# Performance work log

Measured on AMD Instinct MI355X. Metric: run time of the kernel, lower is better.

The kernel has to match this reference:

```python
import jax, jax.numpy as jnp
import numpy as np

B, NQ, HW, D, H = 4, 100, 4096, 1024, 16
HD = D // H  # head dim = 64
EPS = 1e-5
NEG = -1e9


def layernorm(x, g, b):
    mu = jnp.mean(x, axis=-1, keepdims=True)
    var = jnp.mean(jnp.square(x - mu), axis=-1, keepdims=True)
    return (x - mu) * jax.lax.rsqrt(var + EPS) * g + b


def setup_inputs() -> dict:
    key = jax.random.key(0)
    ks = jax.random.split(key, 6)
    scale = 0.02
    return {
        "q": jax.random.normal(ks[0], (B, NQ, D), dtype=jnp.float32),
        "kv": jax.random.normal(ks[1], (B, HW, D), dtype=jnp.float32),
        "mask": jax.random.randint(ks[2], (B, NQ, HW), 0, 2, dtype=jnp.int32),
        "in_proj_w": scale * jax.random.normal(ks[3], (3 * D, D), dtype=jnp.float32),
        "in_proj_b": jnp.zeros((3 * D,), dtype=jnp.float32),
        "out_w": scale * jax.random.normal(ks[4], (D, D), dtype=jnp.float32),
        "out_b": jnp.zeros((D,), dtype=jnp.float32),
        "g_q": jnp.ones((D,), dtype=jnp.float32),
        "b_q": jnp.zeros((D,), dtype=jnp.float32),
        "g_kv": jnp.ones((D,), dtype=jnp.float32),
        "b_kv": jnp.zeros((D,), dtype=jnp.float32),
    }


def reference(q, kv, mask, in_proj_w, in_proj_b, out_w, out_b, g_q, b_q, g_kv, b_kv):
    qn = layernorm(q, g_q, b_q)      # [B,NQ,D]
    kvn = layernorm(kv, g_kv, b_kv)  # [B,HW,D]

    # nn.MultiheadAttention fused in-projection: rows [Wq; Wk; Wv]
    Wq, Wk, Wv = jnp.split(in_proj_w, 3, axis=0)
    bq, bk, bv = jnp.split(in_proj_b, 3, axis=0)
    qp = (qn @ Wq.T + bq).reshape(B, NQ, H, HD)
    kp = (kvn @ Wk.T + bk).reshape(B, HW, H, HD)
    vp = (kvn @ Wv.T + bv).reshape(B, HW, H, HD)

    scores = jnp.einsum("bqhd,bkhd->bhqk", qp, kp) / jnp.sqrt(jnp.float32(HD))

    # Per-query key mask; a query with an all-zero mask attends everywhere
    # (original code sets key_padding_mask=None when kpm.all()).
    allowed = mask.astype(bool)                                   # [B,NQ,HW]
    has_any = jnp.any(allowed, axis=-1, keepdims=True)
    eff = jnp.where(has_any, allowed, True)
    scores = jnp.where(eff[:, None, :, :], scores, NEG)

    attn = jax.nn.softmax(scores, axis=-1)                        # [B,H,NQ,HW]
    ctx = jnp.einsum("bhqk,bkhd->bqhd", attn, vp).reshape(B, NQ, D)
    return ctx @ out_w.T + out_b
```

## Files before the change

### kernel.cpp

```cpp
#include <hip/hip_runtime.h>
#include <math.h>
#include <stdint.h>

#define B_    4
#define NQ_   100
#define HW_   4096
#define D_    1024
#define H_    16
#define HD_   64
#define NCH_  2
#define KCH_  (HW_/NCH_)
#define NT_   (KCH_/128)
#define QT_   32
#define MP_   512

typedef __attribute__((ext_vector_type(8))) short short8;
typedef __attribute__((ext_vector_type(8))) unsigned short ushort8v;
typedef __attribute__((ext_vector_type(4))) float f32x4;

__device__ __forceinline__ unsigned short f2bf(float f) {
    unsigned int u = __float_as_uint(f);
    u += 0x7fffu + ((u >> 16) & 1u);
    return (unsigned short)(u >> 16);
}
__device__ __forceinline__ float bf2f(unsigned short h) {
    return __uint_as_float(((unsigned int)h) << 16);
}

__device__ __forceinline__ void gl2lds16(const void* g, void* l) {
    typedef __attribute__((address_space(1))) unsigned int gu32;
    typedef __attribute__((address_space(3))) unsigned int lu32;
    __builtin_amdgcn_global_load_lds(
        reinterpret_cast<gu32*>(reinterpret_cast<uintptr_t>(g)),
        reinterpret_cast<lu32*>(reinterpret_cast<uintptr_t>(l)),
        16, 0, 0);
}

#define VMCNT0() asm volatile("s_waitcnt vmcnt(0)" ::: "memory")
#define BARRIER() do { __builtin_amdgcn_s_barrier(); \
                       __builtin_amdgcn_sched_barrier(0); } while (0)

__device__ __forceinline__ void ln_row(
    const float* __restrict__ x, const float* __restrict__ g,
    const float* __restrict__ be, unsigned short* __restrict__ y,
    int row, int real_rows, int lane)
{
    unsigned short* yr = y + (size_t)row * D_;
    if (row >= real_rows) {
        #pragma unroll
        for (int k = 0; k < 4; ++k)
            *reinterpret_cast<ushort4*>(yr + lane*4 + k*256) = make_ushort4(0,0,0,0);
        return;
    }
    const float* xr = x + (size_t)row * D_;
    float4 v[4];
    float s = 0.f, ss = 0.f;
    #pragma unroll
    for (int k = 0; k < 4; ++k) {
        v[k] = *reinterpret_cast<const float4*>(xr + lane*4 + k*256);
        s  += v[k].x + v[k].y + v[k].z + v[k].w;
        ss += v[k].x*v[k].x + v[k].y*v[k].y + v[k].z*v[k].z + v[k].w*v[k].w;
    }
    #pragma unroll
    for (int o = 1; o < 64; o <<= 1) {
        s  += __shfl_xor(s,  o);
        ss += __shfl_xor(ss, o);
    }
    const float mu = s * (1.0f / D_);
    const float rs = rsqrtf(ss * (1.0f / D_) - mu*mu + 1e-5f);
    #pragma unroll
    for (int k = 0; k < 4; ++k) {
        const float4 gg = *reinterpret_cast<const float4*>(g  + lane*4 + k*256);
        const float4 bb = *reinterpret_cast<const float4*>(be + lane*4 + k*256);
        ushort4 o;
        o.x = f2bf((v[k].x - mu) * rs * gg.x + bb.x);
        o.y = f2bf((v[k].y - mu) * rs * gg.y + bb.y);
        o.z = f2bf((v[k].z - mu) * rs * gg.z + bb.z);
        o.w = f2bf((v[k].w - mu) * rs * gg.w + bb.w);
        *reinterpret_cast<ushort4*>(yr + lane*4 + k*256) = o;
    }
}

__global__ __launch_bounds__(256) void prep_kernel(
    const float* __restrict__ kv,   const float* __restrict__ g_kv,
    const float* __restrict__ b_kv, unsigned short* __restrict__ kvn,
    const float* __restrict__ qf,   const float* __restrict__ g_q,
    const float* __restrict__ b_q,  unsigned short* __restrict__ qn,
    const float* __restrict__ in_w, unsigned short* __restrict__ wfull,
    const float* __restrict__ out_w, unsigned short* __restrict__ wout,
    const int* __restrict__ mask,   unsigned int* __restrict__ mp)
{
    __shared__ int red[4];
    const int bid = blockIdx.x, tid = threadIdx.x;

    if (bid < 4096) {
        ln_row(kv, g_kv, b_kv, kvn, bid*4 + (tid >> 6), B_*HW_, tid & 63);
    } else if (bid < 7168) {
        const int i = (bid - 4096)*256 + tid;
        const float4 v = reinterpret_cast<const float4*>(in_w)[i];
        ushort4 o;
        o.x = f2bf(v.x); o.y = f2bf(v.y); o.z = f2bf(v.z); o.w = f2bf(v.w);
        reinterpret_cast<ushort4*>(wfull)[i] = o;
    } else if (bid < 8192) {
        const int row = bid - 7168;
        const float4 v = reinterpret_cast<const float4*>(out_w + (size_t)row * D_)[tid];
        ushort4 hi, lo;
        hi.x = f2bf(v.x); hi.y = f2bf(v.y); hi.z = f2bf(v.z); hi.w = f2bf(v.w);
        lo.x = f2bf(v.x - bf2f(hi.x)); lo.y = f2bf(v.y - bf2f(hi.y));
        lo.z = f2bf(v.z - bf2f(hi.z)); lo.w = f2bf(v.w - bf2f(hi.w));
        unsigned short* yr = wout + (size_t)row * 3072;
        reinterpret_cast<ushort4*>(yr)[tid]        = hi;
        reinterpret_cast<ushort4*>(yr + 1024)[tid] = hi;
        reinterpret_cast<ushort4*>(yr + 2048)[tid] = lo;
    } else if (bid < 8704) {
        const int mblk = bid - 8192;
        const int qrow = mblk & 127, mb = mblk >> 7;
        unsigned int word = 0;
        if (qrow < NQ_ && tid < 128) {
            const int4* mr = reinterpret_cast<const int4*>(
                mask + ((size_t)(mb*NQ_ + qrow))*HW_ + tid*32);
            #pragma unroll
            for (int j = 0; j < 8; ++j) {
                const int4 v = mr[j];
                word |= (v.x!=0 ? 1u:0u) << (4*j);
                word |= (v.y!=0 ? 1u:0u) << (4*j+1);
                word |= (v.z!=0 ? 1u:0u) << (4*j+2);
                word |= (v.w!=0 ? 1u:0u) << (4*j+3);
            }
        }
        const int wany = __any(word != 0) ? 1 : 0;
        if ((tid & 63) == 0) red[tid >> 6] = wany;
        __syncthreads();
        const int hasany = red[0] | red[1] | red[2] | red[3];
        if (tid < 128)
            mp[((size_t)(mb*128 + qrow))*128 + tid] = hasany ? word : 0xFFFFFFFFu;
    } else {
        ln_row(qf, g_q, b_q, qn, (bid - 8704)*4 + (tid >> 6), B_*NQ_, tid & 63);
    }
}

__global__ __launch_bounds__(512, 4) void gemm_kv_kernel(
    const unsigned short* __restrict__ A, const unsigned short* __restrict__ Wb,
    const float* __restrict__ bias, unsigned short* __restrict__ kp,
    unsigned short* __restrict__ vt,
    const unsigned short* __restrict__ qA, const unsigned short* __restrict__ qW,
    float* __restrict__ P)
{
    extern __shared__ __align__(16) unsigned short lds[];

    const int tid  = threadIdx.x;
    const int wave = tid >> 6;
    const int lane = tid & 63;
    const int lr   = lane & 15, quad = lane >> 4;

    if (blockIdx.x >= 1024) {
        const int bid2 = blockIdx.x - 1024;
        const int bn = bid2 & 15, bm = (bid2 >> 4) & 7, sk = bid2 >> 7;
        unsigned short* As = lds;
        unsigned short* Bs = lds + 2048;

        const int r0 = (tid & 255) >> 2;
        const int xs = (r0 & 3) ^ ((r0 >> 2) & 3);
        const int kc = (tid & 3) ^ xs;
        const unsigned short* ap = qA + (size_t)(bm*64 + r0)*1024 + sk*128 + kc*8;
        const unsigned short* bp = qW + (size_t)(bn*64 + r0)*1024 + sk*128 + kc*8;
        unsigned short* asd = As + (wave & 3)*512;
        unsigned short* bsd = Bs + (wave & 3)*512;

        f32x4 acc[4];
        #pragma unroll
        for (int j = 0; j < 4; ++j) acc[j] = (f32x4){0.f,0.f,0.f,0.f};

        const int arow = (wave & 3)*16 + lr;
        const int xa = (arow & 3) ^ ((arow >> 2) & 3);
        const int aoff = (arow*4 + (quad ^ xa))*8;
        int boff[4];
        #pragma unroll
        for (int j = 0; j < 4; ++j) {
            const int brow = j*16 + lr;
            const int xb = (brow & 3) ^ ((brow >> 2) & 3);
            boff[j] = (brow*4 + (quad ^ xb))*8;
        }

        #pragma unroll 1
        for (int s = 0; s < 4; ++s) {
            if (tid < 256) { gl2lds16(ap, asd); gl2lds16(bp, bsd); }
            ap += 32; bp += 32;
            __syncthreads();
            if (tid < 256) {
                const short8 af = *reinterpret_cast<const short8*>(&As[aoff]);
                short8 bf[4];
                #pragma unroll
                for (int j = 0; j < 4; ++j)
                    bf[j] = *reinterpret_cast<const short8*>(&Bs[boff[j]]);
                #pragma unroll
                for (int j = 0; j < 4; ++j)
                    acc[j] = __builtin_amdgcn_mfma_f32_16x16x32_bf16(af, bf[j], acc[j], 0, 0, 0);
            }
            __syncthreads();
        }

        if (tid < 256) {
            float* Pb = P + ((size_t)sk*MP_ + bm*64)*1024 + bn*64;
            const int m0 = (wave & 3)*16 + quad*4;
            #pragma unroll
            for (int j = 0; j < 4; ++j)
                #pragma unroll
                for (int r = 0; r < 4; ++r)
                    Pb[(size_t)(m0 + r)*1024 + j*16 + lr] = acc[j][r];
        }
        return;
    }

    const int wm2  = wave >> 2;
    const int wn4  = wave & 3;

    const int x  = blockIdx.x & 7;
    const int g  = blockIdx.x >> 3;
    const int bm = x*16 + (g >> 3);
    const int bn = g & 7;

    const int srow = tid >> 2;
    const int sswz = (srow & 3) ^ ((srow >> 2) & 3);
    const int scol = ((tid & 3) ^ sswz) * 8;
    const unsigned short* aSrc  = A  + (size_t)(bm*128 + srow)*D_ + scol;
    const unsigned short* bSrc0 = Wb + (size_t)(bn*256 + srow)*D_ + scol;
    const unsigned short* bSrc1 = bSrc0 + (size_t)128*D_;
    const int wdst = wave * 512;

    int aoff[4], boff[4];
    #pragma unroll
    for (int fm = 0; fm < 4; ++fm) {
        const int row = wm2*64 + fm*16 + lr;
        aoff[fm] = row*32 + (quad ^ (row & 3) ^ ((row >> 2) & 3))*8;
    }
    #pragma unroll
    for (int fn = 0; fn < 4; ++fn) {
        const int row = wn4*64 + fn*16 + lr;
        boff[fn] = 4096 + row*32 + (quad ^ (row & 3) ^ ((row >> 2) & 3))*8;
    }

    f32x4 acc[4][4];
    #pragma unroll
    for (int i = 0; i < 4; ++i)
        #pragma unroll
        for (int j = 0; j < 4; ++j)
            acc[i][j] = (f32x4){0.f, 0.f, 0.f, 0.f};

    gl2lds16(aSrc,  lds +        wdst);
    gl2lds16(bSrc0, lds + 4096 + wdst);
    gl2lds16(bSrc1, lds + 8192 + wdst);
    aSrc += 32; bSrc0 += 32; bSrc1 += 32;
    VMCNT0();
    BARRIER();

    int cur = 0;
    #pragma unroll 1
    for (int t = 0; t < 32; ++t) {
        const unsigned short* Sl = lds + cur*12288;
        unsigned short*       S2 = lds + (cur ^ 1)*12288;
        short8 afr[4], bfr[4];

        #pragma unroll
        for (int fm = 0; fm < 4; ++fm)
            afr[fm] = *reinterpret_cast<const short8*>(&Sl[aoff[fm]]);
        bfr[0] = *reinterpret_cast<const short8*>(&Sl[boff[0]]);
        bfr[1] = *reinterpret_cast<const short8*>(&Sl[boff[1]]);
        if (t < 31) {
            gl2lds16(aSrc,  S2 +        wdst);
            gl2lds16(bSrc0, S2 + 4096 + wdst);
        }
        __builtin_amdgcn_s_setprio(1);
        #pragma unroll
        for (int fm = 0; fm < 4; ++fm)
            #pragma unroll
            for (int fn = 0; fn < 2; ++fn)
                acc[fm][fn] = __builtin_amdgcn_mfma_f32_16x16x32_bf16(
                    afr[fm], bfr[fn], acc[fm][fn], 0, 0, 0);
        __builtin_amdgcn_s_setprio(0);

        bfr[2] = *reinterpret_cast<const short8*>(&Sl[boff[2]]);
        bfr[3] = *reinterpret_cast<const short8*>(&Sl[boff[3]]);
        if (t < 31) {
            gl2lds16(bSrc1, S2 + 8192 + wdst);
            aSrc += 32; bSrc0 += 32; bSrc1 += 32;
        }
        __builtin_amdgcn_s_setprio(1);
        #pragma unroll
        for (int fm = 0; fm < 4; ++fm)
            #pragma unroll
            for (int fn = 2; fn < 4; ++fn)
                acc[fm][fn] = __builtin_amdgcn_mfma_f32_16x16x32_bf16(
                    afr[fm], bfr[fn], acc[fm][fn], 0, 0, 0);
        __builtin_amdgcn_s_setprio(0);

        VMCNT0();
        BARRIER();
        cur ^= 1;
    }

    const int colbase = bn*256 + wn4*64 + lr;
    const int mbase   = bm*128 + wm2*64 + quad*4;
    if (bn < 4) {
        #pragma unroll
        for (int fn = 0; fn < 4; ++fn) {
            const int n = colbase + fn*16;
            const float bb = bias[n];
            #pragma unroll
            for (int fm = 0; fm < 4; ++fm) {
                unsigned short* Cp = kp + (size_t)(mbase + fm*16)*1024 + n;
                #pragma unroll
                for (int r = 0; r < 4; ++r)
                    Cp[(size_t)r * 1024] = f2bf(acc[fm][fn][r] + bb);
            }
        }
    } else {
        const int b = bm >> 5;
        const int key0 = mbase - b*4096;
        #pragma unroll
        for (int fn = 0; fn < 4; ++fn) {
            const int n = colbase + fn*16;
            const float bb = bias[n];
            unsigned short* vrow = vt + (size_t)(b*1024 + n - 1024) * HW_;
            #pragma unroll
            for (int fm = 0; fm < 4; ++fm) {
                ushort4 o;
                o.x = f2bf(acc[fm][fn][0] + bb);
                o.y = f2bf(acc[fm][fn][1] + bb);
                o.z = f2bf(acc[fm][fn][2] + bb);
                o.w = f2bf(acc[fm][fn][3] + bb);
                *reinterpret_cast<ushort4*>(vrow + key0 + fm*16) = o;
            }
        }
    }
}

__global__ __launch_bounds__(256) void gemm_splitk_kernel(
    const unsigned short* __restrict__ A, const unsigned short* __restrict__ W,
    float* __restrict__ P, int K, int KS)
{
    __shared__ __align__(16) unsigned short As[2048];
    __shared__ __align__(16) unsigned short Bs[2048];
    const int tid = threadIdx.x;
    const int wave = tid >> 6, lane = tid & 63;
    const int lr = lane & 15, quad = lane >> 4;
    const int bn = blockIdx.x, bm = blockIdx.y, sk = blockIdx.z;

    const int r0 = tid >> 2;
    const int xs = (r0 & 3) ^ ((r0 >> 2) & 3);
    const int kc = (tid & 3) ^ xs;
    const unsigned short* ap = A + (size_t)(bm*64 + r0)*K + sk*KS + kc*8;
    const unsigned short* bp = W + (size_t)(bn*64 + r0)*K + sk*KS + kc*8;
    unsigned short* asd = As + wave*512;
    unsigned short* bsd = Bs + wave*512;

    f32x4 acc[4];
    #pragma unroll
    for (int j = 0; j < 4; ++j) acc[j] = (f32x4){0.f,0.f,0.f,0.f};

    const int arow = wave*16 + lr;
    const int xa = (arow & 3) ^ ((arow >> 2) & 3);
    const int aoff = (arow*4 + (quad ^ xa))*8;
    int boff[4];
    #pragma unroll
    for (int j = 0; j < 4; ++j) {
        const int brow = j*16 + lr;
        const int xb = (brow & 3) ^ ((brow >> 2) & 3);
        boff[j] = (brow*4 + (quad ^ xb))*8;
    }

    const int nsteps = KS >> 5;
    for (int s = 0; s < nsteps; ++s) {
        gl2lds16(ap, asd); gl2lds16(bp, bsd);
        ap += 32; bp += 32;
        __syncthreads();
        const short8 af = *reinterpret_cast<const short8*>(&As[aoff]);
        short8 bf[4];
        #pragma unroll
        for (int j = 0; j < 4; ++j)
            bf[j] = *reinterpret_cast<const short8*>(&Bs[boff[j]]);
        #pragma unroll
        for (int j = 0; j < 4; ++j)
            acc[j] = __builtin_amdgcn_mfma_f32_16x16x32_bf16(af, bf[j], acc[j], 0, 0, 0);
        __syncthreads();
    }

    float* Pb = P + ((size_t)sk*MP_ + bm*64)*1024 + bn*64;
    const int m0 = wave*16 + quad*4;
    #pragma unroll
    for (int j = 0; j < 4; ++j)
        #pragma unroll
        for (int r = 0; r < 4; ++r)
            Pb[(size_t)(m0 + r)*1024 + j*16 + lr] = acc[j][r];
}

__global__ __launch_bounds__(256) void reduce_kernel(
    const float* __restrict__ P, const float* __restrict__ bias,
    float* __restrict__ Cout, int SK)
{
    const int i4 = blockIdx.x * 256 + threadIdx.x;
    const int c4 = i4 & 255;
    float4 s = reinterpret_cast<const float4*>(bias)[c4];
    for (int sk = 0; sk < SK; ++sk) {
        const float4 p = reinterpret_cast<const float4*>(P + (size_t)sk*MP_*1024)[i4];
        s.x += p.x; s.y += p.y; s.z += p.z; s.w += p.w;
    }
    reinterpret_cast<float4*>(Cout)[i4] = s;
}

__global__ __launch_bounds__(256) void flash_kernel(
    const float* __restrict__ qp, const unsigned short* __restrict__ kp,
    const unsigned short* __restrict__ vt, const unsigned int* __restrict__ mpack,
    float* __restrict__ partO, float* __restrict__ partL)
{
    __shared__ __align__(16) unsigned char smem[49152];
    unsigned short* Ks  = (unsigned short*)smem;
    unsigned short* Vts = (unsigned short*)(smem + 16384);
    unsigned short* Qs  = (unsigned short*)(smem + 32768);
    unsigned short* Ps  = (unsigned short*)(smem + 37376);
    unsigned int*   MWs = (unsigned int*)  (smem + 47616);
    float*          mlW = (float*)         (smem + 48128);
    float*          Om  = (float*)smem;

    const int tid = threadIdx.x;
    const int wave = tid >> 6, lane = tid & 63;
    const int lr = lane & 15, quad = lane >> 4;

    const int CPX  = (4*H_*B_*NCH_) / 8;
    const int bid  = blockIdx.x;
    const int orig = (bid & 7) * CPX + (bid >> 3);
    const int qt   = orig & 3;
    const int rest = orig >> 2;
    const int h    = rest % H_;
    const int zz   = rest / H_;
    const int b    = zz / NCH_, ks = zz % NCH_;
    const int kb0 = ks * KCH_;

    {
        const int q = tid >> 3, dc = (tid & 7) * 8;
        const int qg = qt*QT_ + q;
        float4 v0 = make_float4(0.f,0.f,0.f,0.f), v1 = v0;
        if (qg < NQ_) {
            const float* src = qp + ((size_t)(b*NQ_ + qg))*D_ + h*HD_ + dc;
            v0 = *reinterpret_cast<const float4*>(src);
            v1 = *reinterpret_cast<const float4*>(src + 4);
        }
        ushort8v o;
        o[0]=f2bf(v0.x*0.125f); o[1]=f2bf(v0.y*0.125f);
        o[2]=f2bf(v0.z*0.125f); o[3]=f2bf(v0.w*0.125f);
        o[4]=f2bf(v1.x*0.125f); o[5]=f2bf(v1.y*0.125f);
        o[6]=f2bf(v1.z*0.125f); o[7]=f2bf(v1.w*0.125f);
        *reinterpret_cast<ushort8v*>(&Qs[q*72 + dc]) = o;
    }

    const unsigned short* kptr[4];
    const unsigned short* vptr[4];
    #pragma unroll
    for (int i = 0; i < 4; ++i) {
        const int s = i*256 + tid;
        const int key = s >> 3, jg = (s & 7) ^ (key & 7);
        kptr[i] = kp + ((size_t)(b*HW_) + kb0 + key)*1024 + h*HD_ + jg*8;
        const int d = s >> 4, js = s & 15, jg2 = js ^ (d & 15);
        vptr[i] = vt + ((size_t)(b*1024 + h*HD_ + d))*HW_ + kb0 + jg2*8;
    }

    int koff[2][2], voff[4];
    #pragma unroll
    for (int kj = 0; kj < 2; ++kj)
        #pragma unroll
        for (int ds = 0; ds < 2; ++ds) {
            const int key_l = wave*32 + kj*16 + lr;
            const int jg = ds*4 + quad;
            koff[kj][ds] = (key_l*8 + (jg ^ (key_l & 7))) * 8;
        }
    #pragma unroll
    for (int dj = 0; dj < 4; ++dj) {
        const int d_l = dj*16 + lr;
        const int jg = wave*4 + quad;
        voff[dj] = (d_l*16 + (jg ^ (d_l & 15))) * 8;
    }

    float lreg[8];
    #pragma unroll
    for (int i = 0; i < 8; ++i) lreg[i] = 0.f;
    f32x4 Ov[2][4];
    #pragma unroll
    for (int i = 0; i < 2; ++i)
        #pragma unroll
        for (int j = 0; j < 4; ++j)
            Ov[i][j] = (f32x4){0.f,0.f,0.f,0.f};

    for (int kt = 0; kt < NT_; ++kt) {
        __syncthreads();
        #pragma unroll
        for (int i = 0; i < 4; ++i) {
            gl2lds16(kptr[i], Ks  + (i*256 + wave*64)*8);
            gl2lds16(vptr[i], Vts + (i*256 + wave*64)*8);
            kptr[i] += 128*1024; vptr[i] += 128;
        }
        if (tid < 128) {
            const int mw = tid >> 5, mq = tid & 31;
            MWs[mw*32 + mq] = mpack[((size_t)(b*128 + qt*QT_ + mq))*128 +
                                    (ks*(KCH_/32) + kt*4 + mw)];
        }
        __syncthreads();

        f32x4 S[2][2];
        #pragma unroll
        for (int i = 0; i < 2; ++i)
            #pragma unroll
            for (int kj = 0; kj < 2; ++kj)
                S[i][kj] = (f32x4){0.f,0.f,0.f,0.f};
        #pragma unroll
        for (int ds = 0; ds < 2; ++ds) {
            short8 aq[2], bk[2];
            aq[0] = *reinterpret_cast<const short8*>(&Qs[(     lr)*72 + ds*32 + quad*8]);
            aq[1] = *reinterpret_cast<const short8*>(&Qs[(16 + lr)*72 + ds*32 + quad*8]);
            bk[0] = *reinterpret_cast<const short8*>(&Ks[koff[0][ds]]);
            bk[1] = *reinterpret_cast<const short8*>(&Ks[koff[1][ds]]);
            #pragma unroll
            for (int i = 0; i < 2; ++i)
                #pragma unroll
                for (int kj = 0; kj < 2; ++kj)
                    S[i][kj] = __builtin_amdgcn_mfma_f32_16x16x32_bf16(
                        aq[i], bk[kj], S[i][kj], 0, 0, 0);
        }

        #pragma unroll
        for (int i = 0; i < 2; ++i) {
            #pragma unroll
            for (int r = 0; r < 4; ++r) {
                const int q = i*16 + quad*4 + r;
                const unsigned int mw = MWs[wave*32 + q];
                const float p0 = ((mw >> lr) & 1u)        ? __expf(S[i][0][r]) : 0.f;
                const float p1 = ((mw >> (16 + lr)) & 1u) ? __expf(S[i][1][r]) : 0.f;
                lreg[i*4+r] += p0 + p1;
                const float p0n = __shfl_xor(p0, 1);
                const float p1n = __shfl_xor(p1, 1);
                if (!(lr & 1)) {
                    const unsigned int w0 = (unsigned)f2bf(p0) | ((unsigned)f2bf(p0n) << 16);
                    const unsigned int w1 = (unsigned)f2bf(p1) | ((unsigned)f2bf(p1n) << 16);
                    *reinterpret_cast<unsigned int*>(&Ps[wave*1280 + q*40 + lr])      = w0;
                    *reinterpret_cast<unsigned int*>(&Ps[wave*1280 + q*40 + 16 + lr]) = w1;
                }
            }
        }

        short8 pf[2], vf[4];
        #pragma unroll
        for (int i = 0; i < 2; ++i)
            pf[i] = *reinterpret_cast<const short8*>(&Ps[wave*1280 + (i*16+lr)*40 + quad*8]);
        #pragma unroll
        for (int dj = 0; dj < 4; ++dj)
            vf[dj] = *reinterpret_cast<const short8*>(&Vts[voff[dj]]);
        #pragma unroll
        for (int i = 0; i < 2; ++i)
            #pragma unroll
            for (int dj = 0; dj < 4; ++dj)
                Ov[i][dj] = __builtin_amdgcn_mfma_f32_16x16x32_bf16(
                    pf[i], vf[dj], Ov[i][dj], 0, 0, 0);
    }

    __syncthreads();
    #pragma unroll
    for (int i = 0; i < 2; ++i)
        #pragma unroll
        for (int r = 0; r < 4; ++r) {
            float l = lreg[i*4+r];
            #pragma unroll
            for (int o = 1; o < 16; o <<= 1) l += __shfl_xor(l, o);
            if (lr == 0) mlW[wave*32 + i*16 + quad*4 + r] = l;
        }
    #pragma unroll
    for (int i = 0; i < 2; ++i)
        #pragma unroll
        for (int dj = 0; dj < 4; ++dj)
            #pragma unroll
            for (int r = 0; r < 4; ++r) {
                const int q = i*16 + quad*4 + r;
                Om[wave*2112 + q*66 + dj*16 + lr] = Ov[i][dj][r];
            }
    __syncthreads();
    {
        const int q = tid >> 3, dc = (tid & 7) * 8;
        float L = 0.f;
        #pragma unroll
        for (int w = 0; w < 4; ++w) L += mlW[w*32 + q];
        float os[8] = {};
        #pragma unroll
        for (int w = 0; w < 4; ++w)
            #pragma unroll
            for (int j = 0; j < 8; ++j)
                os[j] += Om[w*2112 + q*66 + dc + j];
        const size_t pr = (((size_t)(b*H_ + h))*NCH_ + ks)*128 + qt*QT_ + q;
        *reinterpret_cast<float4*>(&partO[pr*HD_ + dc])     = make_float4(os[0],os[1],os[2],os[3]);
        *reinterpret_cast<float4*>(&partO[pr*HD_ + dc + 4]) = make_float4(os[4],os[5],os[6],os[7]);
        if ((tid & 7) == 0) partL[pr] = L;
    }
}

__global__ __launch_bounds__(256) void hilo_a_kernel(
    const float* __restrict__ partO, const float* __restrict__ partL,
    unsigned short* __restrict__ y)
{
    const int row = blockIdx.x;
    const int tid = threadIdx.x;
    unsigned short* yr = y + (size_t)row * 3072;
    if (row >= B_*NQ_) {
        const ushort4 z = make_ushort4(0,0,0,0);
        reinterpret_cast<ushort4*>(yr)[tid]        = z;
        reinterpret_cast<ushort4*>(yr + 1024)[tid] = z;
        reinterpret_cast<ushort4*>(yr + 2048)[tid] = z;
        return;
    }
    const int b = row / NQ_, qi = row % NQ_;
    const int h = tid >> 4, d4 = (tid & 15) * 4;
    float4 O = make_float4(0.f, 0.f, 0.f, 0.f);
    float L = 0.f;
    #pragma unroll
    for (int i = 0; i < NCH_; ++i) {
        const size_t pr = (((size_t)(b*H_ + h))*NCH_ + i)*128 + qi;
        const float4 p = *reinterpret_cast<const float4*>(partO + pr*HD_ + d4);
        O.x += p.x; O.y += p.y; O.z += p.z; O.w += p.w;
        L += partL[pr];
    }
    const float ri = 1.0f / L;
    const float4 v = make_float4(O.x*ri, O.y*ri, O.z*ri, O.w*ri);
    ushort4 hi, lo;
    hi.x = f2bf(v.x); hi.y = f2bf(v.y); hi.z = f2bf(v.z); hi.w = f2bf(v.w);
    lo.x = f2bf(v.x - bf2f(hi.x)); lo.y = f2bf(v.y - bf2f(hi.y));
    lo.z = f2bf(v.z - bf2f(hi.z)); lo.w = f2bf(v.w - bf2f(hi.w));
    reinterpret_cast<ushort4*>(yr)[tid]        = hi;
    reinterpret_cast<ushort4*>(yr + 1024)[tid] = lo;
    reinterpret_cast<ushort4*>(yr + 2048)[tid] = hi;
}

extern "C" void kernel_launch(void* const* d_in, const int* in_sizes, int n_in,
                              void* d_out, int out_size, void* d_ws, size_t ws_size,
                              hipStream_t stream)
{
    const float* q     = (const float*)d_in[0];
    const float* kv    = (const float*)d_in[1];
    const int*   mask  = (const int*)  d_in[2];
    const float* in_w  = (const float*)d_in[3];
    const float* in_b  = (const float*)d_in[4];
    const float* out_w = (const float*)d_in[5];
    const float* out_b = (const float*)d_in[6];
    const float* g_q   = (const float*)d_in[7];
    const float* b_q   = (const float*)d_in[8];
    const float* g_kv  = (const float*)d_in[9];
    const float* b_kv  = (const float*)d_in[10];
    float* out = (float*)d_out;

    char* ws = (char*)d_ws;
    float*          qp       = (float*)         (ws + 0);
    unsigned int*   mpackp   = (unsigned int*)  (ws + 1638400);
    unsigned short* wfull_bf = (unsigned short*)(ws + 1900544);
    unsigned short* qn_bf    = (unsigned short*)(ws + 8192000);
    unsigned short* ctx_cat  = (unsigned short*)(ws + 9240576);
    unsigned short* wout_cat = (unsigned short*)(ws + 12386304);
    float*          P        = (float*)         (ws + 18677760);
    float*          partL    = (float*)         (ws + 37093376);
    float*          partO    = (float*)         (ws + 37355520);
    unsigned short* kvn_bf   = (unsigned short*)(ws + 54132736);
    unsigned short* kp       = (unsigned short*)(ws + 87687168);
    unsigned short* vt       = (unsigned short*)(ws + 121241600);

    static bool attr_set = false;
    if (!attr_set) {
        hipFuncSetAttribute(reinterpret_cast<const void*>(gemm_kv_kernel),
                            hipFuncAttributeMaxDynamicSharedMemorySize, 49152);
        attr_set = true;
    }

    prep_kernel<<<8832, 256, 0, stream>>>(
        kv, g_kv, b_kv, kvn_bf,
        q,  g_q,  b_q,  qn_bf,
        in_w, wfull_bf,
        out_w, wout_cat,
        mask, mpackp);

    gemm_kv_kernel<<<dim3(2048), 512, 49152, stream>>>(
        kvn_bf, wfull_bf + (size_t)D_*D_, in_b + D_, kp, vt,
        qn_bf, wfull_bf, P);
    reduce_kernel<<<B_*NQ_*D_/4/256, 256, 0, stream>>>(P, in_b, qp, 8);

    flash_kernel<<<dim3(4*H_*B_*NCH_), 256, 0, stream>>>(
        qp, kp, vt, mpackp, partO, partL);

    hilo_a_kernel<<<MP_, 256, 0, stream>>>(partO, partL, ctx_cat);
    gemm_splitk_kernel<<<dim3(D_/64, MP_/64, 8), 256, 0, stream>>>(
        ctx_cat, wout_cat, P, 3*D_, 384);
    reduce_kernel<<<B_*NQ_*D_/4/256, 256, 0, stream>>>(P, out_b, out, 8);
}
```

Baseline: 276.6 us.

## Move out_w and mask packing into GEMM kernel; register-prefetch K/V tiles in flash

The out_w hi/lo bf16 split and the mask bit-packing work move from the prep kernel into extra blocks of the KV GEMM launch, so they run alongside GEMM blocks instead of lengthening the prep pass. In the flash kernel, the async global-to-LDS copies are replaced by loading the next K/V tile and mask word into registers while the current tile is computed, then storing them to LDS at the top of each iteration. This is meant to hide global-load latency behind the MFMA work. The cost is higher register pressure, and the extra light blocks in a 512-thread GEMM launch leave most of their threads idle.

```diff
diff --git a/kernel.cpp b/kernel.cpp
--- a/kernel.cpp
+++ b/kernel.cpp
@@ -86,11 +86,8 @@
     const float* __restrict__ b_kv, unsigned short* __restrict__ kvn,
     const float* __restrict__ qf,   const float* __restrict__ g_q,
     const float* __restrict__ b_q,  unsigned short* __restrict__ qn,
-    const float* __restrict__ in_w, unsigned short* __restrict__ wfull,
-    const float* __restrict__ out_w, unsigned short* __restrict__ wout,
-    const int* __restrict__ mask,   unsigned int* __restrict__ mp)
+    const float* __restrict__ in_w, unsigned short* __restrict__ wfull)
 {
-    __shared__ int red[4];
     const int bid = blockIdx.x, tid = threadIdx.x;
 
     if (bid < 4096) {
@@ -101,19 +98,30 @@
         ushort4 o;
         o.x = f2bf(v.x); o.y = f2bf(v.y); o.z = f2bf(v.z); o.w = f2bf(v.w);
         reinterpret_cast<ushort4*>(wfull)[i] = o;
-    } else if (bid < 8192) {
-        const int row = bid - 7168;
-        const float4 v = reinterpret_cast<const float4*>(out_w + (size_t)row * D_)[tid];
-        ushort4 hi, lo;
-        hi.x = f2bf(v.x); hi.y = f2bf(v.y); hi.z = f2bf(v.z); hi.w = f2bf(v.w);
-        lo.x = f2bf(v.x - bf2f(hi.x)); lo.y = f2bf(v.y - bf2f(hi.y));
-        lo.z = f2bf(v.z - bf2f(hi.z)); lo.w = f2bf(v.w - bf2f(hi.w));
-        unsigned short* yr = wout + (size_t)row * 3072;
-        reinterpret_cast<ushort4*>(yr)[tid]        = hi;
-        reinterpret_cast<ushort4*>(yr + 1024)[tid] = hi;
-        reinterpret_cast<ushort4*>(yr + 2048)[tid] = lo;
-    } else if (bid < 8704) {
-        const int mblk = bid - 8192;
+    } else {
+        ln_row(qf, g_q, b_q, qn, (bid - 7168)*4 + (tid >> 6), B_*NQ_, tid & 63);
+    }
+}
+
+__global__ __launch_bounds__(512, 4) void gemm_kv_kernel(
+    const unsigned short* __restrict__ A, const unsigned short* __restrict__ Wb,
+    const float* __restrict__ bias, unsigned short* __restrict__ kp,
+    unsigned short* __restrict__ vt,
+    const unsigned short* __restrict__ qA, const unsigned short* __restrict__ qW,
+    float* __restrict__ P,
+    const float* __restrict__ out_w, unsigned short* __restrict__ wout,
+    const int* __restrict__ mask, unsigned int* __restrict__ mp)
+{
+    extern __shared__ __align__(16) unsigned short lds[];
+
+    const int tid  = threadIdx.x;
+    const int wave = tid >> 6;
+    const int lane = tid & 63;
+    const int lr   = lane & 15, quad = lane >> 4;
+
+    if (blockIdx.x >= 3072) {
+        int* red = (int*)lds;
+        const int mblk = blockIdx.x - 3072;
         const int qrow = mblk & 127, mb = mblk >> 7;
         unsigned int word = 0;
         if (qrow < NQ_ && tid < 128) {
@@ -129,30 +137,30 @@
             }
         }
         const int wany = __any(word != 0) ? 1 : 0;
-        if ((tid & 63) == 0) red[tid >> 6] = wany;
+        if (lane == 0) red[wave] = wany;
         __syncthreads();
-        const int hasany = red[0] | red[1] | red[2] | red[3];
+        int hasany = 0;
+        #pragma unroll
+        for (int w = 0; w < 8; ++w) hasany |= red[w];
         if (tid < 128)
             mp[((size_t)(mb*128 + qrow))*128 + tid] = hasany ? word : 0xFFFFFFFFu;
-    } else {
-        ln_row(qf, g_q, b_q, qn, (bid - 8704)*4 + (tid >> 6), B_*NQ_, tid & 63);
-    }
-}
-
-__global__ __launch_bounds__(512, 4) void gemm_kv_kernel(
-    const unsigned short* __restrict__ A, const unsigned short* __restrict__ Wb,
-    const float* __restrict__ bias, unsigned short* __restrict__ kp,
-    unsigned short* __restrict__ vt,
-    const unsigned short* __restrict__ qA, const unsigned short* __restrict__ qW,
-    float* __restrict__ P)
-{
-    extern __shared__ __align__(16) unsigned short lds[];
-
-    const int tid  = threadIdx.x;
-    const int wave = tid >> 6;
-    const int lane = tid & 63;
-    const int lr   = lane & 15, quad = lane >> 4;
-
+        return;
+    }
+    if (blockIdx.x >= 2048) {
+        if (tid < 256) {
+            const int row = blockIdx.x - 2048;
+            const float4 v = reinterpret_cast<const float4*>(out_w + (size_t)row * D_)[tid];
+            ushort4 hi, lo;
+            hi.x = f2bf(v.x); hi.y = f2bf(v.y); hi.z = f2bf(v.z); hi.w = f2bf(v.w);
+            lo.x = f2bf(v.x - bf2f(hi.x)); lo.y = f2bf(v.y - bf2f(hi.y));
+            lo.z = f2bf(v.z - bf2f(hi.z)); lo.w = f2bf(v.w - bf2f(hi.w));
+            unsigned short* yr = wout + (size_t)row * 3072;
+            reinterpret_cast<ushort4*>(yr)[tid]        = hi;
+            reinterpret_cast<ushort4*>(yr + 1024)[tid] = hi;
+            reinterpret_cast<ushort4*>(yr + 2048)[tid] = lo;
+        }
+        return;
+    }
     if (blockIdx.x >= 1024) {
         const int bid2 = blockIdx.x - 1024;
         const int bn = bid2 & 15, bm = (bid2 >> 4) & 7, sk = bid2 >> 7;
@@ -490,19 +498,33 @@
         for (int j = 0; j < 4; ++j)
             Ov[i][j] = (f32x4){0.f,0.f,0.f,0.f};
 
+    ushort8v kreg[4], vreg[4];
+    unsigned int mreg = 0;
+    #define LOADREG(kt_)                                                      \
+        do {                                                                  \
+            _Pragma("unroll")                                                 \
+            for (int i = 0; i < 4; ++i) {                                     \
+                kreg[i] = *reinterpret_cast<const ushort8v*>(kptr[i]);        \
+                vreg[i] = *reinterpret_cast<const ushort8v*>(vptr[i]);        \
+                kptr[i] += 128*1024; vptr[i] += 128;                          \
+            }                                                                 \
+            if (tid < 128)                                                    \
+                mreg = mpack[((size_t)(b*128 + qt*QT_ + (tid & 31)))*128 +    \
+                             (ks*(KCH_/32) + (kt_)*4 + (tid >> 5))];          \
+        } while (0)
+
+    LOADREG(0);
+
+    #pragma unroll 1
     for (int kt = 0; kt < NT_; ++kt) {
         __syncthreads();
         #pragma unroll
         for (int i = 0; i < 4; ++i) {
-            gl2lds16(kptr[i], Ks  + (i*256 + wave*64)*8);
-            gl2lds16(vptr[i], Vts + (i*256 + wave*64)*8);
-            kptr[i] += 128*1024; vptr[i] += 128;
-        }
-        if (tid < 128) {
-            const int mw = tid >> 5, mq = tid & 31;
-            MWs[mw*32 + mq] = mpack[((size_t)(b*128 + qt*QT_ + mq))*128 +
-                                    (ks*(KCH_/32) + kt*4 + mw)];
-        }
+            *reinterpret_cast<ushort8v*>(Ks  + (i*256 + tid)*8) = kreg[i];
+            *reinterpret_cast<ushort8v*>(Vts + (i*256 + tid)*8) = vreg[i];
+        }
+        if (tid < 128) MWs[(tid >> 5)*32 + (tid & 31)] = mreg;
+        if (kt + 1 < NT_) LOADREG(kt + 1);
         __syncthreads();
 
         f32x4 S[2][2];
@@ -560,6 +582,7 @@
                 Ov[i][dj] = __builtin_amdgcn_mfma_f32_16x16x32_bf16(
                     pf[i], vf[dj], Ov[i][dj], 0, 0, 0);
     }
+    #undef LOADREG
 
     __syncthreads();
     #pragma unroll
@@ -673,16 +696,15 @@
         attr_set = true;
     }
 
-    prep_kernel<<<8832, 256, 0, stream>>>(
+    prep_kernel<<<7296, 256, 0, stream>>>(
         kv, g_kv, b_kv, kvn_bf,
         q,  g_q,  b_q,  qn_bf,
-        in_w, wfull_bf,
-        out_w, wout_cat,
-        mask, mpackp);
-
-    gemm_kv_kernel<<<dim3(2048), 512, 49152, stream>>>(
+        in_w, wfull_bf);
+
+    gemm_kv_kernel<<<dim3(3584), 512, 49152, stream>>>(
         kvn_bf, wfull_bf + (size_t)D_*D_, in_b + D_, kp, vt,
-        qn_bf, wfull_bf, P);
+        qn_bf, wfull_bf, P,
+        out_w, wout_cat, mask, mpackp);
     reduce_kernel<<<B_*NQ_*D_/4/256, 256, 0, stream>>>(P, in_b, qp, 8);
 
     flash_kernel<<<dim3(4*H_*B_*NCH_), 256, 0, stream>>>(
```

Result: no change. 278.6 us (+0.7%).
